# Performance work log

Hardware: AMD Instinct MI355X
Metric: run time of the kernel (lower is better)

## Reference

```python
import jax, jax.numpy as jnp
import numpy as np

B, S, D, H, HZ = 4096, 64, 9, 128, 32
DT = 0.1


def _lstm_cell(x, h, c, Wih, Whh, bih, bhh):
    gates = x @ Wih.T + bih + h @ Whh.T + bhh
    i, f, g, o = jnp.split(gates, 4, axis=-1)
    c_new = jax.nn.sigmoid(f) * c + jax.nn.sigmoid(i) * jnp.tanh(g)
    h_new = jax.nn.sigmoid(o) * jnp.tanh(c_new)
    return h_new, c_new


def _forward(input_batch, W_ih_enc, W_hh_enc, b_ih_enc, b_hh_enc, W_e, V_e, v_e,
             W_d, V_d, v_d, W_ih_dec, W_hh_dec, b_ih_dec, b_hh_dec,
             W_out, b_out, scaler_mean, scaler_std, pos_mean):
    bsz = input_batch.shape[0]
    # ---- encoder with input attention ----
    x_perm = jnp.swapaxes(input_batch, 1, 2)          # (B, D, S)
    attn_input = jnp.einsum('bds,ts->bdt', x_perm, V_e)  # V_e * x^i, precomputed once
    h0 = jnp.zeros((bsz, H), input_batch.dtype)
    c0 = jnp.zeros((bsz, H), input_batch.dtype)

    def enc_step(carry, x_t):
        h, c = carry
        attn_hidden = jnp.concatenate([h, c], axis=1) @ W_e.T          # (B, S)
        comb = jnp.tanh(attn_hidden[:, None, :] + attn_input)          # (B, D, S)
        e = comb @ v_e                                                 # (B, D)
        alpha = jax.nn.softmax(e, axis=1)
        h, c = _lstm_cell(alpha * x_t, h, c, W_ih_enc, W_hh_enc, b_ih_enc, b_hh_enc)
        return (h, c), h

    (h_enc, c_enc), hs = jax.lax.scan(enc_step, (h0, c0), jnp.swapaxes(input_batch, 0, 1))
    enc_hidden = jnp.swapaxes(hs, 0, 1)               # (B, S, H)
    attn_encoder = enc_hidden @ V_d.T                 # V_d * h_j, precomputed once

    # ---- initial physics state ----
    pos = input_batch[:, -1, :3] + pos_mean
    vel = input_batch[:, -1, 3:6] * scaler_std + scaler_mean
    pre_vel = input_batch[:, -2, 3:6] * scaler_std + scaler_mean
    acc = (vel - pre_vel) / DT

    def dec_step(carry, _):
        d, c, pos, vel, acc = carry
        attn_dec = jnp.concatenate([d, c], axis=1) @ W_d.T             # (B, H)
        comb = jnp.tanh(attn_dec[:, None, :] + attn_encoder)           # (B, S, H)
        beta = jax.nn.softmax(comb @ v_d, axis=1)                      # (B, S)
        context = jnp.einsum('bs,bsh->bh', beta, enc_hidden)           # (B, H)
        phys = jnp.concatenate([pos - pos_mean,
                                (vel - scaler_mean) / scaler_std,
                                acc / scaler_std], axis=1)             # (B, 9)
        d, c = _lstm_cell(jnp.concatenate([phys, context], axis=1), d, c,
                          W_ih_dec, W_hh_dec, b_ih_dec, b_hh_dec)
        pred_acc = (jnp.concatenate([d, context], axis=1) @ W_out.T + b_out) * scaler_std
        pos_pred = pos + vel * DT + 0.5 * acc * DT * DT                # Verlet position
        vel_new = vel + 0.5 * (acc + pred_acc) * DT                    # Verlet velocity
        out = jnp.concatenate([pos_pred, vel_new, pred_acc], axis=1)   # (B, 9)
        return (d, c, pos_pred, vel_new, pred_acc), out

    _, outs = jax.lax.scan(dec_step, (h_enc, c_enc, pos, vel, acc), None, length=HZ)
    return jnp.swapaxes(outs, 0, 1)                   # (B, HZ, 9)


def setup_inputs() -> dict:
    key = jax.random.key(0)
    ks = jax.random.split(key, 16)
    p = lambda k, shape, s=0.05: jax.random.normal(k, shape, dtype=jnp.float32) * s
    return dict(
        input_batch=jax.random.normal(ks[0], (B, S, D), dtype=jnp.float32),
        W_ih_enc=p(ks[1], (4 * H, D)), W_hh_enc=p(ks[2], (4 * H, H)),
        b_ih_enc=jnp.zeros((4 * H,), jnp.float32), b_hh_enc=jnp.zeros((4 * H,), jnp.float32),
        W_e=p(ks[3], (S, 2 * H)), V_e=p(ks[4], (S, S)), v_e=p(ks[5], (S,)),
        W_d=p(ks[6], (H, 2 * H)), V_d=p(ks[7], (H, H)), v_d=p(ks[8], (H,)),
        W_ih_dec=p(ks[9], (4 * H, 9 + H)), W_hh_dec=p(ks[10], (4 * H, H)),
        b_ih_dec=jnp.zeros((4 * H,), jnp.float32), b_hh_dec=jnp.zeros((4 * H,), jnp.float32),
        W_out=p(ks[11], (3, 2 * H)), b_out=jnp.zeros((3,), jnp.float32),
        scaler_mean=p(ks[12], (3,), 0.1),
        scaler_std=jnp.abs(p(ks[13], (3,), 0.1)) + 1.0,
        pos_mean=p(ks[14], (3,), 0.1),
    )


def reference(input_batch, W_ih_enc, W_hh_enc, b_ih_enc, b_hh_enc, W_e, V_e, v_e,
              W_d, V_d, v_d, W_ih_dec, W_hh_dec, b_ih_dec, b_hh_dec,
              W_out, b_out, scaler_mean, scaler_std, pos_mean):
    return _forward(input_batch, W_ih_enc, W_hh_enc, b_ih_enc, b_hh_enc, W_e, V_e, v_e,
                    W_d, V_d, v_d, W_ih_dec, W_hh_dec, b_ih_dec, b_hh_dec,
                    W_out, b_out, scaler_mean, scaler_std, pos_mean)
```

## Files before the change

kernel.cpp:

```cpp
#include <hip/hip_runtime.h>
#include <hip/hip_bf16.h>
#include <hip/hip_fp8.h>

#define B_   4096
#define S_   64
#define D_   9
#define H_   128
#define HZ_  32
#define DT_  0.1f

#define OFF_WET    0
#define OFF_VET    16384
#define OFF_WENCT  20480
#define OFF_BENC   90624
#define OFF_WDT    91136
#define OFF_WDECT  123904
#define OFF_BDEC   259584
#define OFF_WOUTT  260096
#define OFF_VDT    260864
#define OFF_DECD   277248
#define OFF_DECC   801536
#define F32_TOTAL  1325824
#define PREP_N     277248

typedef __bf16 bf16x8 __attribute__((ext_vector_type(8)));
typedef float  f32x4  __attribute__((ext_vector_type(4)));
typedef float  f32x2  __attribute__((ext_vector_type(2)));

__device__ __forceinline__ float fast_tanh(float x) {
    float e = __expf(2.0f * x);
    return 1.0f - __fdividef(2.0f, e + 1.0f);
}
__device__ __forceinline__ float sigf(float x) {
    return __fdividef(1.0f, 1.0f + __expf(-x));
}
__device__ __forceinline__ float bf_lo(unsigned int u) { return __uint_as_float(u << 16); }
__device__ __forceinline__ float bf_hi(unsigned int u) { return __uint_as_float(u & 0xffff0000u); }
__device__ __forceinline__ float bfu2f(unsigned short u) { return __uint_as_float((unsigned int)u << 16); }
__device__ __forceinline__ unsigned short f2bfu(float f) {
    __hip_bfloat16 b = __float2bfloat16(f);
    return *(unsigned short*)&b;
}
__device__ __forceinline__ unsigned int pack_bf(float lo, float hi) {
    return (unsigned int)f2bfu(lo) | ((unsigned int)f2bfu(hi) << 16);
}
__device__ __forceinline__ float f8tof(unsigned int byte) {
    __hip_fp8_e4m3 t; t.__x = (unsigned char)byte; return (float)t;
}
__device__ __forceinline__ unsigned char f2f8(float f) {
    __hip_fp8_e4m3 q(f); return q.__x;
}
__device__ __forceinline__ unsigned int pack4_f8(float a, float b, float c, float d) {
    return (unsigned int)f2f8(a) | ((unsigned int)f2f8(b) << 8) |
           ((unsigned int)f2f8(c) << 16) | ((unsigned int)f2f8(d) << 24);
}
template<bool HI>
__device__ __forceinline__ f32x2 cvt2f8(unsigned int u) {
    return __builtin_amdgcn_cvt_pk_f32_fp8(u, HI);
}

__global__ void prep_kernel(const float* __restrict__ Wih_e, const float* __restrict__ Whh_e,
    const float* __restrict__ bih_e, const float* __restrict__ bhh_e,
    const float* __restrict__ W_e, const float* __restrict__ V_e,
    const float* __restrict__ W_d, const float* __restrict__ V_d,
    const float* __restrict__ Wih_d, const float* __restrict__ Whh_d,
    const float* __restrict__ bih_d, const float* __restrict__ bhh_d,
    const float* __restrict__ W_out, float* __restrict__ ws) {
  for (int idx = blockIdx.x * blockDim.x + threadIdx.x; idx < PREP_N;
       idx += gridDim.x * blockDim.x) {
    int i = idx;
    if (i < 16384) { continue; }
    i -= 16384;
    if (i < 4096) { int s = i >> 6, t = i & 63; ws[OFF_VET + i] = V_e[t * 64 + s]; continue; }
    i -= 4096;
    if (i < 70144) { continue; }
    i -= 70144;
    if (i < 512) { ws[OFF_BENC + i] = bih_e[i] + bhh_e[i]; continue; }
    i -= 512;
    if (i < 32768) { continue; }
    i -= 32768;
    if (i < 135680) { continue; }
    i -= 135680;
    if (i < 512) { ws[OFF_BDEC + i] = bih_d[i] + bhh_d[i]; continue; }
    i -= 512;
    if (i < 768) { int k = i / 3, j = i % 3; ws[OFF_WOUTT + i] = W_out[j * 256 + k]; continue; }
  }
}

__global__ void prep_mfma_kernel(const float* __restrict__ W_d,
    const float* __restrict__ Wih_d, const float* __restrict__ Whh_d,
    unsigned short* __restrict__ WdTm, unsigned short* __restrict__ WdecTm) {
  int idx = blockIdx.x * blockDim.x + threadIdx.x;
  if (idx < 32768) {
    int j = idx & 7, l = (idx >> 3) & 63, t = idx >> 9;
    int nt = t & 7, ks = t >> 3;
    int k = ks * 32 + (l >> 4) * 8 + j;
    int n = nt * 16 + (l & 15);
    WdTm[idx] = f2bfu(W_d[n * 256 + k]);
    return;
  }
  int i2 = idx - 32768;
  if (i2 < 147456) {
    int j = i2 & 7, l = (i2 >> 3) & 63, t = i2 >> 9;
    int ks = t % 9, tile = t / 9;
    int q = tile & 3, is = tile >> 2;
    int k = ks * 32 + (l >> 4) * 8 + j;
    int g = q * 128 + is * 16 + (l & 15);
    float v;
    if (k < 128)      v = Whh_d[g * 128 + k];
    else if (k < 256) v = Wih_d[g * 137 + 9 + (k - 128)];
    else if (k < 265) v = Wih_d[g * 137 + (k - 256)];
    else              v = 0.f;
    WdecTm[i2] = f2bfu(v);
  }
}

__global__ void prep_enc_mfma_kernel(const float* __restrict__ W_e,
    const float* __restrict__ Wih_e, const float* __restrict__ Whh_e,
    const float* __restrict__ V_d,
    unsigned short* __restrict__ WeTm, unsigned short* __restrict__ WencTm,
    unsigned short* __restrict__ VdTm) {
  int idx = blockIdx.x * blockDim.x + threadIdx.x;
  if (idx < 16384) {
    int j = idx & 7, l = (idx >> 3) & 63, tile = idx >> 9;
    int nt = tile & 3, ks = tile >> 2;
    int k = ks * 32 + (l >> 4) * 8 + j;
    int n = nt * 16 + (l & 15);
    WeTm[idx] = f2bfu(W_e[n * 256 + k]);
    return;
  }
  int i2 = idx - 16384;
  if (i2 < 81920) {
    int j = i2 & 7, l = (i2 >> 3) & 63, tile = i2 >> 9;
    int ks = tile % 5, tq = tile / 5;
    int q = tq & 3, is = tq >> 2;
    int kk = (l >> 4) * 8 + j;
    int g = q * 128 + is * 16 + (l & 15);
    float v;
    if (ks < 4) v = Whh_e[g * 128 + ks * 32 + kk];
    else        v = (kk < 9) ? Wih_e[g * 9 + kk] : 0.f;
    WencTm[i2] = f2bfu(v);
    return;
  }
  int i3 = i2 - 81920;
  if (i3 < 16384) {
    int j = i3 & 7, l = (i3 >> 3) & 63, tile = i3 >> 9;
    int nt = tile & 7, ks = tile >> 3;
    int i = ks * 32 + (l >> 4) * 8 + j;
    int n = nt * 16 + (l & 15);
    VdTm[i3] = f2bfu(V_d[n * 128 + i]);
  }
}

__global__ __launch_bounds__(512, 1) void encoder_mfma_kernel(
    const float* __restrict__ x_in, const float* __restrict__ ws,
    const float* __restrict__ v_e_g,
    const unsigned short* __restrict__ WeTm, const unsigned short* __restrict__ WencTm,
    __hip_bfloat16* __restrict__ EH,
    unsigned short* __restrict__ dG, float* __restrict__ cG) {
  __shared__ unsigned short hA[2][16 * 296];
  __shared__ float cF[16 * 132];
  __shared__ float ahL[16 * 64];
  __shared__ unsigned short aiL[16 * 576];
  __shared__ unsigned short xbL[16 * 576];

  const int tid = threadIdx.x;
  const int b0 = blockIdx.x * 16;
  const int l = tid & 63, w = tid >> 6;
  const int quad = l >> 4, l15 = l & 15;

  for (int i = tid; i < 16 * 576; i += 512) {
    int m = i / 576, r = i % 576;
    xbL[i] = f2bfu(x_in[(size_t)(b0 + m) * 576 + r]);
  }
  for (int i = tid; i < 2 * 16 * 296; i += 512) ((unsigned short*)hA)[i] = 0;
  for (int i = tid; i < 16 * 132; i += 512) cF[i] = 0.f;
  __syncthreads();

  {
    const float* __restrict__ VeT = ws + OFF_VET;
    for (int i = tid; i < 16 * 576; i += 512) {
      int t = i & 63, dd = (i >> 6) % 9, m = i / 576;
      float acc = 0.f;
      for (int s = 0; s < 64; ++s) acc += bfu2f(xbL[m * 576 + s * 9 + dd]) * VeT[s * 64 + t];
      aiL[m * 576 + dd * 64 + t] = f2bfu(acc);
    }
  }
  const float ve_r = v_e_g[l];
  const int ig = w * 16 + l15;
  float bbq[4];
  #pragma unroll
  for (int q = 0; q < 4; ++q) bbq[q] = ws[OFF_BENC + q * 128 + ig];
  __syncthreads();

  for (int t = 0; t < S_; ++t) {
    unsigned short* bufC = hA[t & 1];
    unsigned short* bufN = hA[(t + 1) & 1];
    if (w < 4) {
      f32x4 acc = {0.f, 0.f, 0.f, 0.f};
      #pragma unroll
      for (int ks = 0; ks < 8; ++ks) {
        uint4 au = *(const uint4*)&bufC[l15 * 296 + ks * 32 + quad * 8];
        uint4 bu = *(const uint4*)(WeTm + (size_t)((ks * 4 + w) * 64 + l) * 8);
        acc = __builtin_amdgcn_mfma_f32_16x16x32_bf16(
            __builtin_bit_cast(bf16x8, au), __builtin_bit_cast(bf16x8, bu), acc, 0, 0, 0);
      }
      #pragma unroll
      for (int r = 0; r < 4; ++r)
        ahL[(quad * 4 + r) * 64 + w * 16 + l15] = acc[r];
    }
    __syncthreads();
    {
      const int m0 = 2 * w, m1 = 2 * w + 1;
      float a0 = ahL[m0 * 64 + l], a1 = ahL[m1 * 64 + l];
      float e0k = -1e30f, e1k = -1e30f;
      #pragma unroll
      for (int dd = 0; dd < 9; ++dd) {
        float t0 = fast_tanh(a0 + bfu2f(aiL[m0 * 576 + dd * 64 + l])) * ve_r;
        float t1 = fast_tanh(a1 + bfu2f(aiL[m1 * 576 + dd * 64 + l])) * ve_r;
        #pragma unroll
        for (int off = 32; off; off >>= 1) {
          t0 += __shfl_xor(t0, off, 64);
          t1 += __shfl_xor(t1, off, 64);
        }
        if (l == dd) { e0k = t0; e1k = t1; }
      }
      float mx0 = e0k, mx1 = e1k;
      #pragma unroll
      for (int off = 8; off; off >>= 1) {
        mx0 = fmaxf(mx0, __shfl_xor(mx0, off, 64));
        mx1 = fmaxf(mx1, __shfl_xor(mx1, off, 64));
      }
      float ex0 = (l < 9) ? __expf(e0k - mx0) : 0.f;
      float ex1 = (l < 9) ? __expf(e1k - mx1) : 0.f;
      float s0 = ex0, s1 = ex1;
      #pragma unroll
      for (int off = 8; off; off >>= 1) {
        s0 += __shfl_xor(s0, off, 64);
        s1 += __shfl_xor(s1, off, 64);
      }
      if (l < 9) {
        bufC[m0 * 296 + 256 + l] = f2bfu(__fdividef(ex0, s0) * bfu2f(xbL[m0 * 576 + t * 9 + l]));
        bufC[m1 * 296 + 256 + l] = f2bfu(__fdividef(ex1, s1) * bfu2f(xbL[m1 * 576 + t * 9 + l]));
      }
    }
    __syncthreads();
    {
      uint4 af[5];
      #pragma unroll
      for (int ks = 0; ks < 4; ++ks)
        af[ks] = *(const uint4*)&bufC[l15 * 296 + ks * 32 + quad * 8];
      af[4] = *(const uint4*)&bufC[l15 * 296 + 256 + quad * 8];
      f32x4 g4[4];
      #pragma unroll
      for (int q = 0; q < 4; ++q) {
        f32x4 acc = {0.f, 0.f, 0.f, 0.f};
        #pragma unroll
        for (int ks = 0; ks < 5; ++ks) {
          uint4 bu = *(const uint4*)(WencTm + (size_t)(((w * 4 + q) * 5 + ks) * 64 + l) * 8);
          acc = __builtin_amdgcn_mfma_f32_16x16x32_bf16(
              __builtin_bit_cast(bf16x8, af[ks]), __builtin_bit_cast(bf16x8, bu), acc, 0, 0, 0);
        }
        g4[q] = acc;
      }
      #pragma unroll
      for (int r = 0; r < 4; ++r) {
        int m = quad * 4 + r;
        float gi = g4[0][r] + bbq[0];
        float gf = g4[1][r] + bbq[1];
        float gg = g4[2][r] + bbq[2];
        float go = g4[3][r] + bbq[3];
        float co = cF[m * 132 + ig];
        float cn = sigf(gf) * co + sigf(gi) * fast_tanh(gg);
        float hn = sigf(go) * fast_tanh(cn);
        cF[m * 132 + ig] = cn;
        bufN[m * 296 + ig] = f2bfu(hn);
        bufN[m * 296 + 128 + ig] = f2bfu(cn);
        EH[((size_t)(b0 + m) * S_ + t) * H_ + ig] = __float2bfloat16(hn);
      }
    }
    __syncthreads();
  }
  for (int i = tid; i < 16 * 128; i += 512) {
    int m = i >> 7, ii = i & 127;
    dG[(size_t)(b0 + m) * 128 + ii] = hA[0][m * 296 + ii];
    cG[(size_t)(b0 + m) * 128 + ii] = cF[m * 132 + ii];
  }
}

__global__ __launch_bounds__(256) void attnenc_mfma_kernel(
    const unsigned short* __restrict__ EH, const unsigned short* __restrict__ VdTm,
    unsigned char* __restrict__ AETf8, unsigned char* __restrict__ EHf8) {
  const int tid = threadIdx.x;
  const int b = blockIdx.x * 4 + (tid >> 6);
  const int l = tid & 63;
  const int quad = l >> 4, l15 = l & 15;

  const unsigned short* ehb = EH + (size_t)b * 8192;
  uint4 A[4][4];
  #pragma unroll
  for (int st = 0; st < 4; ++st)
    #pragma unroll
    for (int ks = 0; ks < 4; ++ks)
      A[st][ks] = *(const uint4*)(ehb + (st * 16 + l15) * 128 + ks * 32 + quad * 8);

  {
    unsigned char* e8b = EHf8 + (size_t)b * 8192;
    #pragma unroll
    for (int st = 0; st < 4; ++st)
      #pragma unroll
      for (int ks = 0; ks < 4; ++ks) {
        uint4 a = A[st][ks];
        uint2 pk;
        pk.x = pack4_f8(bf_lo(a.x), bf_hi(a.x), bf_lo(a.y), bf_hi(a.y));
        pk.y = pack4_f8(bf_lo(a.z), bf_hi(a.z), bf_lo(a.w), bf_hi(a.w));
        *(uint2*)(e8b + (st * 16 + l15) * 128 + ks * 32 + quad * 8) = pk;
      }
  }

  unsigned char* outb = AETf8 + (size_t)b * 8192;
  const int k = l15;
  #pragma unroll
  for (int nt = 0; nt < 8; ++nt) {
    uint4 Bf[4];
    #pragma unroll
    for (int ks = 0; ks < 4; ++ks)
      Bf[ks] = *(const uint4*)(VdTm + (size_t)((ks * 8 + nt) * 64 + l) * 8);
    int kg = nt * 16 + k;
    int kb = kg >> 3, k7 = kg & 7;
    #pragma unroll
    for (int st = 0; st < 4; ++st) {
      f32x4 acc = {0.f, 0.f, 0.f, 0.f};
      #pragma unroll
      for (int ks = 0; ks < 4; ++ks)
        acc = __builtin_amdgcn_mfma_f32_16x16x32_bf16(
            __builtin_bit_cast(bf16x8, A[st][ks]), __builtin_bit_cast(bf16x8, Bf[ks]), acc, 0, 0, 0);
      #pragma unroll
      for (int r = 0; r < 4; ++r) {
        int s = st * 16 + quad * 4 + r;
        outb[kb * 512 + s * 8 + k7] = f2f8(acc[r]);
      }
    }
  }
}

__global__ __launch_bounds__(512, 2) void dec_fused_kernel(
    const float* __restrict__ ws,
    const unsigned char* __restrict__ AETf8, const unsigned char* __restrict__ EHf8,
    const unsigned short* __restrict__ dG, const float* __restrict__ cG,
    const unsigned short* __restrict__ WdTm, const unsigned short* __restrict__ WdecTm,
    const float* __restrict__ v_d_g, const float* __restrict__ b_out_g,
    const float* __restrict__ smean_g, const float* __restrict__ sstd_g,
    const float* __restrict__ pmean_g,
    const float* __restrict__ x_in,
    float* __restrict__ out) {
  __shared__ unsigned char  AET[8][8192];
  __shared__ unsigned char  EHL[8][8192];
  __shared__ unsigned short gA[16 * 296];
  __shared__ unsigned short dcB[16 * 264];
  __shared__ unsigned short adL[8 * 128];
  __shared__ float          bet[8][64];
  __shared__ float          vdL[128];
  __shared__ float          pcs[8 * 3 * 8];
  __shared__ float          pvs[8 * 12];

  const int tid = threadIdx.x;
  const int b0 = blockIdx.x * 8;
  const int l = tid & 63, w = tid >> 6;
  const int quad = l >> 4, l15 = l & 15;
  const int i = w * 16 + l15;

  for (int idx = tid; idx < 16 * 296; idx += 512) gA[idx] = 0;
  for (int idx = tid; idx < 16 * 264; idx += 512) dcB[idx] = 0;
  {
    const uint4* srcA = (const uint4*)(AETf8 + (size_t)b0 * 8192);
    const uint4* srcE = (const uint4*)(EHf8 + (size_t)b0 * 8192);
    uint4* dstA = (uint4*)AET;
    uint4* dstE = (uint4*)EHL;
    for (int idx = tid; idx < 4096; idx += 512) {
      dstA[idx] = srcA[idx];
      dstE[idx] = srcE[idx];
    }
  }
  if (tid < 128) vdL[tid] = v_d_g[tid];
  __syncthreads();

  if (tid < 128) {
    int m = tid >> 4, i0 = (tid & 15) * 8;
    uint4 dv = *(const uint4*)(dG + (size_t)(b0 + m) * 128 + i0);
    *(uint4*)&gA[m * 296 + i0] = dv;
    *(uint4*)&dcB[m * 264 + i0] = dv;
    float4 c0 = *(const float4*)(cG + (size_t)(b0 + m) * 128 + i0);
    float4 c1 = *(const float4*)(cG + (size_t)(b0 + m) * 128 + i0 + 4);
    uint4 pk;
    pk.x = pack_bf(c0.x, c0.y); pk.y = pack_bf(c0.z, c0.w);
    pk.z = pack_bf(c1.x, c1.y); pk.w = pack_bf(c1.z, c1.w);
    *(uint4*)&dcB[m * 264 + 128 + i0] = pk;
  }
  if (tid < 24) {
    int m = tid / 3, jj = tid % 3;
    const float* xi = x_in + (size_t)(b0 + m) * 576;
    float sm = smean_g[jj], ss = sstd_g[jj], pm = pmean_g[jj];
    float v  = xi[63 * 9 + 3 + jj] * ss + sm;
    float pv = xi[62 * 9 + 3 + jj] * ss + sm;
    float pos = xi[63 * 9 + jj] + pm;
    float ac = (v - pv) / DT_;
    float* P = pvs + m * 12;
    P[jj] = pos; P[3 + jj] = v; P[6 + jj] = ac;
    gA[m * 296 + 256 + jj]     = f2bfu(pos - pm);
    gA[m * 296 + 256 + 3 + jj] = f2bfu((v - sm) / ss);
    gA[m * 296 + 256 + 6 + jj] = f2bfu(ac / ss);
  }
  float bb[4];
  #pragma unroll
  for (int q = 0; q < 4; ++q) bb[q] = ws[OFF_BDEC + q * 128 + i];
  float k_sm = 0.f, k_ss = 1.f, k_pm = 0.f, k_bo = 0.f;
  if (tid < 24) {
    int jj = tid % 3;
    k_sm = smean_g[jj]; k_ss = sstd_g[jj]; k_pm = pmean_g[jj]; k_bo = b_out_g[jj];
  }
  float cReg[4];
  #pragma unroll
  for (int r = 0; r < 4; ++r)
    cReg[r] = (quad < 2) ? cG[(size_t)(b0 + quad * 4 + r) * 128 + i] : 0.f;
  __syncthreads();

  {
    const int nt = w;
    f32x4 acc = {0.f, 0.f, 0.f, 0.f};
    #pragma unroll
    for (int ks = 0; ks < 8; ++ks) {
      uint4 au = *(const uint4*)&dcB[l15 * 264 + ks * 32 + quad * 8];
      uint4 bu = *(const uint4*)(WdTm + (size_t)((ks * 8 + nt) * 64 + l) * 8);
      acc = __builtin_amdgcn_mfma_f32_16x16x32_bf16(
          __builtin_bit_cast(bf16x8, au), __builtin_bit_cast(bf16x8, bu), acc, 0, 0, 0);
    }
    if (quad < 2) {
      int n = nt * 16 + l15;
      #pragma unroll
      for (int r = 0; r < 4; ++r) adL[(quad * 4 + r) * 128 + n] = f2bfu(acc[r]);
    }
  }
  __syncthreads();

  for (int hz = 0; hz < HZ_; ++hz) {
    {
      const unsigned char* aet = AET[w];
      const unsigned short* adp = adL + w * 128;
      float e0 = 0.f;
      #pragma unroll
      for (int kb = 0; kb < 16; ++kb) {
        uint2 av = *(const uint2*)(aet + kb * 512 + l * 8);
        uint4 ad8 = *(const uint4*)(adp + kb * 8);
        float4 v0 = *(const float4*)&vdL[kb * 8];
        float4 v1 = *(const float4*)&vdL[kb * 8 + 4];
        f32x2 p0 = cvt2f8<false>(av.x), p1 = cvt2f8<true>(av.x);
        f32x2 p2 = cvt2f8<false>(av.y), p3 = cvt2f8<true>(av.y);
        e0 += fast_tanh(bf_lo(ad8.x) + p0[0]) * v0.x;
        e0 += fast_tanh(bf_hi(ad8.x) + p0[1]) * v0.y;
        e0 += fast_tanh(bf_lo(ad8.y) + p1[0]) * v0.z;
        e0 += fast_tanh(bf_hi(ad8.y) + p1[1]) * v0.w;
        e0 += fast_tanh(bf_lo(ad8.z) + p2[0]) * v1.x;
        e0 += fast_tanh(bf_hi(ad8.z) + p2[1]) * v1.y;
        e0 += fast_tanh(bf_lo(ad8.w) + p3[0]) * v1.z;
        e0 += fast_tanh(bf_hi(ad8.w) + p3[1]) * v1.w;
      }
      float mx = e0;
      #pragma unroll
      for (int off = 32; off; off >>= 1) mx = fmaxf(mx, __shfl_xor(mx, off, 64));
      float ex = __expf(e0 - mx);
      float ss = ex;
      #pragma unroll
      for (int off = 32; off; off >>= 1) ss += __shfl_xor(ss, off, 64);
      bet[w][l] = __fdividef(ex, ss);
    }
    {
      const unsigned char* ehb = EHL[w];
      const int i0 = l15 * 8;
      float a[8];
      #pragma unroll
      for (int r = 0; r < 8; ++r) a[r] = 0.f;
      #pragma unroll
      for (int it = 0; it < 16; ++it) {
        int s = quad * 16 + it;
        uint2 ev = *(const uint2*)(ehb + s * 128 + i0);
        float bt = bet[w][s];
        f32x2 c0 = cvt2f8<false>(ev.x), c1 = cvt2f8<true>(ev.x);
        f32x2 c2 = cvt2f8<false>(ev.y), c3 = cvt2f8<true>(ev.y);
        a[0] += bt * c0[0]; a[1] += bt * c0[1];
        a[2] += bt * c1[0]; a[3] += bt * c1[1];
        a[4] += bt * c2[0]; a[5] += bt * c2[1];
        a[6] += bt * c3[0]; a[7] += bt * c3[1];
      }
      #pragma unroll
      for (int r = 0; r < 8; ++r) {
        a[r] += __shfl_xor(a[r], 16, 64);
        a[r] += __shfl_xor(a[r], 32, 64);
      }
      if (quad == 0) {
        uint4 pk;
        pk.x = pack_bf(a[0], a[1]); pk.y = pack_bf(a[2], a[3]);
        pk.z = pack_bf(a[4], a[5]); pk.w = pack_bf(a[6], a[7]);
        *(uint4*)&gA[w * 296 + 128 + i0] = pk;
      }
    }
    __syncthreads();

    uint4 af[9];
    #pragma unroll
    for (int ks = 0; ks < 9; ++ks)
      af[ks] = *(const uint4*)&gA[l15 * 296 + ks * 32 + quad * 8];
    __syncthreads();

    {
      f32x4 g4[4];
      #pragma unroll
      for (int q = 0; q < 4; ++q) {
        f32x4 acc = {0.f, 0.f, 0.f, 0.f};
        #pragma unroll
        for (int ks = 0; ks < 9; ++ks) {
          uint4 bu = *(const uint4*)(WdecTm + (size_t)(((w * 4 + q) * 9 + ks) * 64 + l) * 8);
          acc = __builtin_amdgcn_mfma_f32_16x16x32_bf16(
              __builtin_bit_cast(bf16x8, af[ks]), __builtin_bit_cast(bf16x8, bu), acc, 0, 0, 0);
        }
        g4[q] = acc;
      }
      if (quad < 2) {
        #pragma unroll
        for (int r = 0; r < 4; ++r) {
          int m = quad * 4 + r;
          float gi = g4[0][r] + bb[0];
          float gf = g4[1][r] + bb[1];
          float gg = g4[2][r] + bb[2];
          float go = g4[3][r] + bb[3];
          float cn = sigf(gf) * cReg[r] + sigf(gi) * fast_tanh(gg);
          float hn = sigf(go) * fast_tanh(cn);
          cReg[r] = cn;
          unsigned short hb = f2bfu(hn);
          gA[m * 296 + i] = hb;
          dcB[m * 264 + i] = hb;
          dcB[m * 264 + 128 + i] = f2bfu(cn);
        }
      }
    }
    __syncthreads();

    {
      const int nt = w;
      f32x4 acc = {0.f, 0.f, 0.f, 0.f};
      #pragma unroll
      for (int ks = 0; ks < 8; ++ks) {
        uint4 au = *(const uint4*)&dcB[l15 * 264 + ks * 32 + quad * 8];
        uint4 bu = *(const uint4*)(WdTm + (size_t)((ks * 8 + nt) * 64 + l) * 8);
        acc = __builtin_amdgcn_mfma_f32_16x16x32_bf16(
            __builtin_bit_cast(bf16x8, au), __builtin_bit_cast(bf16x8, bu), acc, 0, 0, 0);
      }
      if (quad < 2) {
        int n = nt * 16 + l15;
        #pragma unroll
        for (int r = 0; r < 4; ++r) adL[(quad * 4 + r) * 128 + n] = f2bfu(acc[r]);
      }
    }
    if (tid < 192) {
      int m = tid / 24, r2 = tid % 24, jj = r2 >> 3, part = r2 & 7;
      float acc = 0.f;
      #pragma unroll 4
      for (int k = part * 32; k < part * 32 + 32; ++k)
        acc += bfu2f(gA[m * 296 + k]) * ws[OFF_WOUTT + k * 3 + jj];
      pcs[(m * 3 + jj) * 8 + part] = acc;
    }
    __syncthreads();

    if (tid < 24) {
      int m = tid / 3, jj = tid % 3;
      float s = k_bo;
      #pragma unroll
      for (int p = 0; p < 8; ++p) s += pcs[(m * 3 + jj) * 8 + p];
      float pacc = s * k_ss;
      float* P = pvs + m * 12;
      float pos = P[jj], vel = P[3 + jj], ac = P[6 + jj];
      float ppred = pos + vel * DT_ + 0.5f * ac * DT_ * DT_;
      float vnew  = vel + 0.5f * (ac + pacc) * DT_;
      size_t ob = ((size_t)(b0 + m) * HZ_ + hz) * 9;
      out[ob + jj] = ppred; out[ob + 3 + jj] = vnew; out[ob + 6 + jj] = pacc;
      P[jj] = ppred; P[3 + jj] = vnew; P[6 + jj] = pacc;
      gA[m * 296 + 256 + jj]     = f2bfu(ppred - k_pm);
      gA[m * 296 + 256 + 3 + jj] = f2bfu((vnew - k_sm) / k_ss);
      gA[m * 296 + 256 + 6 + jj] = f2bfu(pacc / k_ss);
    }
  }
}

extern "C" void kernel_launch(void* const* d_in, const int* in_sizes, int n_in,
                              void* d_out, int out_size, void* d_ws, size_t ws_size,
                              hipStream_t stream) {
  (void)in_sizes; (void)n_in; (void)out_size; (void)ws_size;
  const float* x      = (const float*)d_in[0];
  const float* Wih_e  = (const float*)d_in[1];
  const float* Whh_e  = (const float*)d_in[2];
  const float* bih_e  = (const float*)d_in[3];
  const float* bhh_e  = (const float*)d_in[4];
  const float* W_e    = (const float*)d_in[5];
  const float* V_e    = (const float*)d_in[6];
  const float* v_e    = (const float*)d_in[7];
  const float* W_d    = (const float*)d_in[8];
  const float* V_d    = (const float*)d_in[9];
  const float* v_d    = (const float*)d_in[10];
  const float* Wih_d  = (const float*)d_in[11];
  const float* Whh_d  = (const float*)d_in[12];
  const float* bih_d  = (const float*)d_in[13];
  const float* bhh_d  = (const float*)d_in[14];
  const float* W_out  = (const float*)d_in[15];
  const float* b_out  = (const float*)d_in[16];
  const float* smean  = (const float*)d_in[17];
  const float* sstd   = (const float*)d_in[18];
  const float* pmean  = (const float*)d_in[19];

  float* ws = (float*)d_ws;
  unsigned short* WeTm   = (unsigned short*)(ws + OFF_WET);
  unsigned short* WencTm = (unsigned short*)(ws + OFF_WENCT);
  unsigned short* WdTm   = (unsigned short*)(ws + OFF_WDT);
  unsigned short* WdecTm = (unsigned short*)(ws + OFF_WDECT);
  unsigned short* VdTm   = (unsigned short*)(ws + OFF_VDT);
  unsigned short* dG     = (unsigned short*)(ws + OFF_DECD);
  float* cG = ws + OFF_DECC;
  unsigned short* ub  = (unsigned short*)(ws + F32_TOTAL);
  unsigned short* EH  = ub;
  unsigned char*  AETf8 = (unsigned char*)(ub + 33554432);
  unsigned char*  EHf8  = AETf8 + (size_t)B_ * 8192;
  float* out = (float*)d_out;

  prep_kernel<<<(PREP_N + 255) / 256, 256, 0, stream>>>(
      Wih_e, Whh_e, bih_e, bhh_e, W_e, V_e, W_d, V_d,
      Wih_d, Whh_d, bih_d, bhh_d, W_out, ws);
  prep_mfma_kernel<<<(32768 + 147456 + 255) / 256, 256, 0, stream>>>(
      W_d, Wih_d, Whh_d, WdTm, WdecTm);
  prep_enc_mfma_kernel<<<(16384 + 81920 + 16384 + 255) / 256, 256, 0, stream>>>(
      W_e, Wih_e, Whh_e, V_d, WeTm, WencTm, VdTm);
  encoder_mfma_kernel<<<B_ / 16, 512, 0, stream>>>(
      x, ws, v_e, WeTm, WencTm, (__hip_bfloat16*)EH, dG, cG);
  attnenc_mfma_kernel<<<B_ / 4, 256, 0, stream>>>(EH, VdTm, AETf8, EHf8);
  dec_fused_kernel<<<B_ / 8, 512, 0, stream>>>(
      ws, AETf8, EHf8, dG, cG, WdTm, WdecTm,
      v_d, b_out, smean, sstd, pmean, x, out);
}
```

Before: 2.002 ms.

## Merge decoder LDS buffers with ping-pong hidden state to drop a barrier

Replaces the two separate LDS operand buffers (gA and dcB) with one shared buffer that double-buffers the hidden state across horizon steps. This removes the per-step register snapshot of A fragments and the __syncthreads that guarded it, and avoids writing the hidden state twice. The gate MFMA loop is reordered so each A fragment is loaded once and reused across the four gates, and the attention-score reduction uses four partial accumulators to shorten the dependency chain. The ping-pong indexing adds complexity and correctness risk.

```diff
diff --git a/kernel.cpp b/kernel.cpp
--- a/kernel.cpp
+++ b/kernel.cpp
@@ -22,6 +22,13 @@
 #define OFF_DECC   801536
 #define F32_TOTAL  1325824
 #define PREP_N     277248
+
+#define DCX_S   552
+#define OF_D0   0
+#define OF_D1   128
+#define OF_C    256
+#define OF_CTX  384
+#define OF_PH   512
 
 typedef __bf16 bf16x8 __attribute__((ext_vector_type(8)));
 typedef float  f32x4  __attribute__((ext_vector_type(4)));
@@ -356,8 +363,7 @@
     float* __restrict__ out) {
   __shared__ unsigned char  AET[8][8192];
   __shared__ unsigned char  EHL[8][8192];
-  __shared__ unsigned short gA[16 * 296];
-  __shared__ unsigned short dcB[16 * 264];
+  __shared__ unsigned short dcx[16 * DCX_S];
   __shared__ unsigned short adL[8 * 128];
   __shared__ float          bet[8][64];
   __shared__ float          vdL[128];
@@ -370,8 +376,7 @@
   const int quad = l >> 4, l15 = l & 15;
   const int i = w * 16 + l15;
 
-  for (int idx = tid; idx < 16 * 296; idx += 512) gA[idx] = 0;
-  for (int idx = tid; idx < 16 * 264; idx += 512) dcB[idx] = 0;
+  for (int idx = tid; idx < 16 * DCX_S; idx += 512) dcx[idx] = 0;
   {
     const uint4* srcA = (const uint4*)(AETf8 + (size_t)b0 * 8192);
     const uint4* srcE = (const uint4*)(EHf8 + (size_t)b0 * 8192);
@@ -388,14 +393,13 @@
   if (tid < 128) {
     int m = tid >> 4, i0 = (tid & 15) * 8;
     uint4 dv = *(const uint4*)(dG + (size_t)(b0 + m) * 128 + i0);
-    *(uint4*)&gA[m * 296 + i0] = dv;
-    *(uint4*)&dcB[m * 264 + i0] = dv;
+    *(uint4*)&dcx[m * DCX_S + OF_D0 + i0] = dv;
     float4 c0 = *(const float4*)(cG + (size_t)(b0 + m) * 128 + i0);
     float4 c1 = *(const float4*)(cG + (size_t)(b0 + m) * 128 + i0 + 4);
     uint4 pk;
     pk.x = pack_bf(c0.x, c0.y); pk.y = pack_bf(c0.z, c0.w);
     pk.z = pack_bf(c1.x, c1.y); pk.w = pack_bf(c1.z, c1.w);
-    *(uint4*)&dcB[m * 264 + 128 + i0] = pk;
+    *(uint4*)&dcx[m * DCX_S + OF_C + i0] = pk;
   }
   if (tid < 24) {
     int m = tid / 3, jj = tid % 3;
@@ -407,9 +411,9 @@
     float ac = (v - pv) / DT_;
     float* P = pvs + m * 12;
     P[jj] = pos; P[3 + jj] = v; P[6 + jj] = ac;
-    gA[m * 296 + 256 + jj]     = f2bfu(pos - pm);
-    gA[m * 296 + 256 + 3 + jj] = f2bfu((v - sm) / ss);
-    gA[m * 296 + 256 + 6 + jj] = f2bfu(ac / ss);
+    dcx[m * DCX_S + OF_PH + jj]     = f2bfu(pos - pm);
+    dcx[m * DCX_S + OF_PH + 3 + jj] = f2bfu((v - sm) / ss);
+    dcx[m * DCX_S + OF_PH + 6 + jj] = f2bfu(ac / ss);
   }
   float bb[4];
   #pragma unroll
@@ -430,7 +434,8 @@
     f32x4 acc = {0.f, 0.f, 0.f, 0.f};
     #pragma unroll
     for (int ks = 0; ks < 8; ++ks) {
-      uint4 au = *(const uint4*)&dcB[l15 * 264 + ks * 32 + quad * 8];
+      int off = (ks < 4) ? (OF_D0 + ks * 32) : (OF_C + (ks - 4) * 32);
+      uint4 au = *(const uint4*)&dcx[l15 * DCX_S + off + quad * 8];
       uint4 bu = *(const uint4*)(WdTm + (size_t)((ks * 8 + nt) * 64 + l) * 8);
       acc = __builtin_amdgcn_mfma_f32_16x16x32_bf16(
           __builtin_bit_cast(bf16x8, au), __builtin_bit_cast(bf16x8, bu), acc, 0, 0, 0);
@@ -444,10 +449,13 @@
   __syncthreads();
 
   for (int hz = 0; hz < HZ_; ++hz) {
+    const int dcur = (hz & 1) ? OF_D1 : OF_D0;
+    const int dnxt = (hz & 1) ? OF_D0 : OF_D1;
+
     {
       const unsigned char* aet = AET[w];
       const unsigned short* adp = adL + w * 128;
-      float e0 = 0.f;
+      float eacc[4] = {0.f, 0.f, 0.f, 0.f};
       #pragma unroll
       for (int kb = 0; kb < 16; ++kb) {
         uint2 av = *(const uint2*)(aet + kb * 512 + l * 8);
@@ -456,15 +464,18 @@
         float4 v1 = *(const float4*)&vdL[kb * 8 + 4];
         f32x2 p0 = cvt2f8<false>(av.x), p1 = cvt2f8<true>(av.x);
         f32x2 p2 = cvt2f8<false>(av.y), p3 = cvt2f8<true>(av.y);
-        e0 += fast_tanh(bf_lo(ad8.x) + p0[0]) * v0.x;
-        e0 += fast_tanh(bf_hi(ad8.x) + p0[1]) * v0.y;
-        e0 += fast_tanh(bf_lo(ad8.y) + p1[0]) * v0.z;
-        e0 += fast_tanh(bf_hi(ad8.y) + p1[1]) * v0.w;
-        e0 += fast_tanh(bf_lo(ad8.z) + p2[0]) * v1.x;
-        e0 += fast_tanh(bf_hi(ad8.z) + p2[1]) * v1.y;
-        e0 += fast_tanh(bf_lo(ad8.w) + p3[0]) * v1.z;
-        e0 += fast_tanh(bf_hi(ad8.w) + p3[1]) * v1.w;
-      }
+        float e = eacc[kb & 3];
+        e += fast_tanh(bf_lo(ad8.x) + p0[0]) * v0.x;
+        e += fast_tanh(bf_hi(ad8.x) + p0[1]) * v0.y;
+        e += fast_tanh(bf_lo(ad8.y) + p1[0]) * v0.z;
+        e += fast_tanh(bf_hi(ad8.y) + p1[1]) * v0.w;
+        e += fast_tanh(bf_lo(ad8.z) + p2[0]) * v1.x;
+        e += fast_tanh(bf_hi(ad8.z) + p2[1]) * v1.y;
+        e += fast_tanh(bf_lo(ad8.w) + p3[0]) * v1.z;
+        e += fast_tanh(bf_hi(ad8.w) + p3[1]) * v1.w;
+        eacc[kb & 3] = e;
+      }
+      float e0 = (eacc[0] + eacc[1]) + (eacc[2] + eacc[3]);
       float mx = e0;
       #pragma unroll
       for (int off = 32; off; off >>= 1) mx = fmaxf(mx, __shfl_xor(mx, off, 64));
@@ -501,29 +512,26 @@
         uint4 pk;
         pk.x = pack_bf(a[0], a[1]); pk.y = pack_bf(a[2], a[3]);
         pk.z = pack_bf(a[4], a[5]); pk.w = pack_bf(a[6], a[7]);
-        *(uint4*)&gA[w * 296 + 128 + i0] = pk;
-      }
-    }
-    __syncthreads();
-
-    uint4 af[9];
-    #pragma unroll
-    for (int ks = 0; ks < 9; ++ks)
-      af[ks] = *(const uint4*)&gA[l15 * 296 + ks * 32 + quad * 8];
+        *(uint4*)&dcx[w * DCX_S + OF_CTX + i0] = pk;
+      }
+    }
     __syncthreads();
 
     {
       f32x4 g4[4];
       #pragma unroll
-      for (int q = 0; q < 4; ++q) {
-        f32x4 acc = {0.f, 0.f, 0.f, 0.f};
+      for (int q = 0; q < 4; ++q) g4[q] = (f32x4){0.f, 0.f, 0.f, 0.f};
+      #pragma unroll
+      for (int ks = 0; ks < 9; ++ks) {
+        int off = (ks < 4) ? (dcur + ks * 32)
+                           : ((ks < 8) ? (OF_CTX + (ks - 4) * 32) : OF_PH);
+        uint4 af = *(const uint4*)&dcx[l15 * DCX_S + off + quad * 8];
         #pragma unroll
-        for (int ks = 0; ks < 9; ++ks) {
+        for (int q = 0; q < 4; ++q) {
           uint4 bu = *(const uint4*)(WdecTm + (size_t)(((w * 4 + q) * 9 + ks) * 64 + l) * 8);
-          acc = __builtin_amdgcn_mfma_f32_16x16x32_bf16(
-              __builtin_bit_cast(bf16x8, af[ks]), __builtin_bit_cast(bf16x8, bu), acc, 0, 0, 0);
+          g4[q] = __builtin_amdgcn_mfma_f32_16x16x32_bf16(
+              __builtin_bit_cast(bf16x8, af), __builtin_bit_cast(bf16x8, bu), g4[q], 0, 0, 0);
         }
-        g4[q] = acc;
       }
       if (quad < 2) {
         #pragma unroll
@@ -536,10 +544,8 @@
           float cn = sigf(gf) * cReg[r] + sigf(gi) * fast_tanh(gg);
           float hn = sigf(go) * fast_tanh(cn);
           cReg[r] = cn;
-          unsigned short hb = f2bfu(hn);
-          gA[m * 296 + i] = hb;
-          dcB[m * 264 + i] = hb;
-          dcB[m * 264 + 128 + i] = f2bfu(cn);
+          dcx[m * DCX_S + dnxt + i] = f2bfu(hn);
+          dcx[m * DCX_S + OF_C + i] = f2bfu(cn);
         }
       }
     }
@@ -550,7 +556,8 @@
       f32x4 acc = {0.f, 0.f, 0.f, 0.f};
       #pragma unroll
       for (int ks = 0; ks < 8; ++ks) {
-        uint4 au = *(const uint4*)&dcB[l15 * 264 + ks * 32 + quad * 8];
+        int off = (ks < 4) ? (dnxt + ks * 32) : (OF_C + (ks - 4) * 32);
+        uint4 au = *(const uint4*)&dcx[l15 * DCX_S + off + quad * 8];
         uint4 bu = *(const uint4*)(WdTm + (size_t)((ks * 8 + nt) * 64 + l) * 8);
         acc = __builtin_amdgcn_mfma_f32_16x16x32_bf16(
             __builtin_bit_cast(bf16x8, au), __builtin_bit_cast(bf16x8, bu), acc, 0, 0, 0);
@@ -563,10 +570,11 @@
     }
     if (tid < 192) {
       int m = tid / 24, r2 = tid % 24, jj = r2 >> 3, part = r2 & 7;
+      int kbase = (part < 4) ? (dnxt + part * 32) : (OF_CTX + (part - 4) * 32);
       float acc = 0.f;
       #pragma unroll 4
-      for (int k = part * 32; k < part * 32 + 32; ++k)
-        acc += bfu2f(gA[m * 296 + k]) * ws[OFF_WOUTT + k * 3 + jj];
+      for (int kk = 0; kk < 32; ++kk)
+        acc += bfu2f(dcx[m * DCX_S + kbase + kk]) * ws[OFF_WOUTT + (part * 32 + kk) * 3 + jj];
       pcs[(m * 3 + jj) * 8 + part] = acc;
     }
     __syncthreads();
@@ -584,9 +592,9 @@
       size_t ob = ((size_t)(b0 + m) * HZ_ + hz) * 9;
       out[ob + jj] = ppred; out[ob + 3 + jj] = vnew; out[ob + 6 + jj] = pacc;
       P[jj] = ppred; P[3 + jj] = vnew; P[6 + jj] = pacc;
-      gA[m * 296 + 256 + jj]     = f2bfu(ppred - k_pm);
-      gA[m * 296 + 256 + 3 + jj] = f2bfu((vnew - k_sm) / k_ss);
-      gA[m * 296 + 256 + 6 + jj] = f2bfu(pacc / k_ss);
+      dcx[m * DCX_S + OF_PH + jj]     = f2bfu(ppred - k_pm);
+      dcx[m * DCX_S + OF_PH + 3 + jj] = f2bfu((vnew - k_sm) / k_ss);
+      dcx[m * DCX_S + OF_PH + 6 + jj] = f2bfu(pacc / k_ss);
     }
   }
 }
```

New measurement: 1.995 ms. About the same (-0.3%).
